# Optimization experiments

Hardware: AMD Instinct MI355X
Metric: run time of the kernel (lower is better)

Reference implementation:

```python
import jax, jax.numpy as jnp
import numpy as np


def setup_inputs() -> dict:
    key = jax.random.key(0)
    ks = jax.random.split(key, 8)
    B, T, V, H = 32, 256, 1024, 1024
    scale_i = 1.0 / np.sqrt(V)   # lecun_normal-style init for dense kernels
    scale_h = 1.0 / np.sqrt(H)
    return {
        "c0": jax.random.normal(ks[0], (B, H), jnp.float32),
        "h0": jax.random.normal(ks[1], (B, H), jnp.float32),
        "inputs": jax.random.normal(ks[2], (B, T, V), jnp.float32),
        "Wi": jax.random.normal(ks[3], (V, 4 * H), jnp.float32) * scale_i,
        "Wh": jax.random.normal(ks[4], (H, 4 * H), jnp.float32) * scale_h,
        "b": jnp.zeros((4 * H,), jnp.float32),
        "Wd": jax.random.normal(ks[5], (H, V), jnp.float32) * scale_h,
        "bd": jnp.zeros((V,), jnp.float32),
    }


def reference(c0, h0, inputs, Wi, Wh, b, Wd, bd):
    # LSTM scanned over time axis (axis=1 of inputs), then Dense -> vocab.
    H = h0.shape[-1]

    def step(carry, x_t):  # x_t: [B, V]
        c, h = carry
        z = x_t @ Wi + h @ Wh + b            # [B, 4H], gates i,f,g,o
        i, f, g, o = jnp.split(z, 4, axis=-1)
        i = jax.nn.sigmoid(i)
        f = jax.nn.sigmoid(f)
        g = jnp.tanh(g)
        o = jax.nn.sigmoid(o)
        c = f * c + i * g
        h = o * jnp.tanh(c)
        return (c, h), h

    xs = jnp.swapaxes(inputs, 0, 1)          # [T, B, V]
    (c, h), hs = jax.lax.scan(step, (c0, h0), xs)
    outputs = jnp.swapaxes(hs, 0, 1)          # [B, T, H]
    x = outputs @ Wd + bd                     # [B, T, V]
    return (c, h, x)
```

## Files before the change

### kernel.cpp

```cpp
#include <hip/hip_runtime.h>
#include <cstdio>

typedef unsigned short u16;
typedef unsigned int u32;
typedef unsigned long long u64;
typedef __attribute__((ext_vector_type(8))) short bf16x8;
typedef __attribute__((ext_vector_type(4))) float f32x4;

#define NWG 128

__device__ inline u16 f2bf(float x) {
  union { float f; unsigned u; } v; v.f = x;
  unsigned r = v.u + 0x7FFFu + ((v.u >> 16) & 1u);
  return (u16)(r >> 16);
}
__device__ inline float sigm(float x) { return 1.0f / (1.0f + __expf(-x)); }
__device__ inline float tanh_fast(float x) { return 1.0f - 2.0f / (__expf(2.0f * x) + 1.0f); }

__global__ __launch_bounds__(256) void k_convert(const float* __restrict__ in,
                                                 u16* __restrict__ out, int n4) {
  int i = blockIdx.x * blockDim.x + threadIdx.x;
  int stride = gridDim.x * blockDim.x;
  const float4* in4 = (const float4*)in;
  ushort4* out4 = (ushort4*)out;
  for (; i < n4; i += stride) {
    float4 v = in4[i];
    ushort4 o; o.x = f2bf(v.x); o.y = f2bf(v.y); o.z = f2bf(v.z); o.w = f2bf(v.w);
    out4[i] = o;
  }
}

__global__ __launch_bounds__(256) void k_init_h(const float* __restrict__ h0,
                                                u16* __restrict__ h_bf,
                                                u32* __restrict__ flags) {
  int i = blockIdx.x * blockDim.x + threadIdx.x;
  if (i < NWG) flags[i] = 0u;
  if (i < 32768) h_bf[i] = f2bf(h0[i]);
}

__global__ __launch_bounds__(256) void k_transpose(const float* __restrict__ in,
                                                   u16* __restrict__ out, int R, int C) {
  __shared__ u16 tile[32][33];
  int tx = threadIdx.x & 31, ty = threadIdx.x >> 5;
  int c = blockIdx.x * 32 + tx;
  for (int i = 0; i < 32; i += 8) {
    int r = blockIdx.y * 32 + ty + i;
    tile[ty + i][tx] = f2bf(in[(size_t)r * C + c]);
  }
  __syncthreads();
  int r = blockIdx.y * 32 + tx;
  for (int i = 0; i < 32; i += 8) {
    int cc = blockIdx.x * 32 + ty + i;
    out[(size_t)cc * R + r] = tile[tx][ty + i];
  }
}

__global__ __launch_bounds__(256) void k_gemm_bt(const u16* __restrict__ A,
                                                 const u16* __restrict__ BT,
                                                 const float* __restrict__ bias,
                                                 float* __restrict__ C,
                                                 int M, int N, int K) {
  __shared__ u16 As[128][40];
  __shared__ u16 Bs[128][40];
  const int m0 = blockIdx.y * 128, n0 = blockIdx.x * 128;
  const int tid = threadIdx.x;
  const int lane = tid & 63, wave = tid >> 6;
  const int wm = (wave >> 1) * 64, wn = (wave & 1) * 64;
  const int lm = lane & 15, quad = lane >> 4;
  const int r = tid >> 1, kh = (tid & 1) * 16;

  f32x4 acc[4][4];
  for (int i = 0; i < 4; i++)
    for (int j = 0; j < 4; j++) acc[i][j] = (f32x4){0.f, 0.f, 0.f, 0.f};

  for (int k0 = 0; k0 < K; k0 += 32) {
    const uint4* ap = (const uint4*)(A + (size_t)(m0 + r) * K + k0 + kh);
    uint4 av0 = ap[0], av1 = ap[1];
    const uint4* bp = (const uint4*)(BT + (size_t)(n0 + r) * K + k0 + kh);
    uint4 bv0 = bp[0], bv1 = bp[1];
    __syncthreads();
    *(uint4*)&As[r][kh] = av0; *(uint4*)&As[r][kh + 8] = av1;
    *(uint4*)&Bs[r][kh] = bv0; *(uint4*)&Bs[r][kh + 8] = bv1;
    __syncthreads();
    bf16x8 a_frag[4], b_frag[4];
    for (int i = 0; i < 4; i++) a_frag[i] = *(const bf16x8*)&As[wm + i * 16 + lm][quad * 8];
    for (int j = 0; j < 4; j++) b_frag[j] = *(const bf16x8*)&Bs[wn + j * 16 + lm][quad * 8];
    for (int i = 0; i < 4; i++)
      for (int j = 0; j < 4; j++)
        acc[i][j] = __builtin_amdgcn_mfma_f32_16x16x32_bf16(a_frag[i], b_frag[j], acc[i][j], 0, 0, 0);
  }
  for (int i = 0; i < 4; i++)
    for (int j = 0; j < 4; j++) {
      int row = m0 + wm + i * 16 + quad * 4;
      int col = n0 + wn + j * 16 + lm;
      float bc = bias[col];
      for (int rr = 0; rr < 4; rr++)
        C[(size_t)(row + rr) * N + col] = acc[i][j][rr] + bc;
    }
}

__global__ __launch_bounds__(256) void k_lstm(const float* __restrict__ Z,
                                              const u16* __restrict__ WhT,
                                              const float* __restrict__ c0,
                                              u16* __restrict__ h_bf,
                                              u16* __restrict__ Hs,
                                              float* __restrict__ out_c,
                                              float* __restrict__ out_h,
                                              u32* __restrict__ flags) {
  __shared__ u16 Whs[32][1032];
  __shared__ u16 h_lds[32][1032];
  __shared__ float z_buf[32][34];
  const int g = blockIdx.x;
  const int tid = threadIdx.x;
  const int lane = tid & 63, wave = tid >> 6;
  const int lm = lane & 15, quad = lane >> 4;
  const int mhalf = wave >> 1, ntile = wave & 1;
  const int b = tid >> 3, jl = tid & 7;

  {
    int pc = tid >> 3, seg = tid & 7;
    int grow = (pc >> 3) * 1024 + 8 * g + (pc & 7);
    const uint4* src = (const uint4*)(WhT + (size_t)grow * 1024 + seg * 128);
#pragma unroll
    for (int i = 0; i < 16; i++) {
      uint4 v = src[i];
      *(uint4*)&Whs[pc][seg * 128 + i * 8] = v;
    }
  }
  float creg = c0[b * 1024 + 8 * g + jl];

  for (int t = 0; t < 256; t++) {
    size_t zbase = ((size_t)b * 256 + t) * 4096 + 8 * g + jl;
    float z_i = Z[zbase], z_f = Z[zbase + 1024], z_g = Z[zbase + 2048], z_o = Z[zbase + 3072];

    {
      const u32 tgt = (u32)t;
      const u32* f0 = flags + lane;
      const u32* f1 = flags + 64 + lane;
      while (true) {
        u32 v0 = __hip_atomic_load(f0, __ATOMIC_RELAXED, __HIP_MEMORY_SCOPE_AGENT);
        u32 v1 = __hip_atomic_load(f1, __ATOMIC_RELAXED, __HIP_MEMORY_SCOPE_AGENT);
        if (__all((v0 >= tgt) && (v1 >= tgt))) break;
        __builtin_amdgcn_s_sleep(1);
      }
      asm volatile("" ::: "memory");
    }

    {
      const u64* hq = (const u64*)(h_bf + (size_t)(t & 1) * 32768);
      u64 v[32];
#pragma unroll
      for (int i = 0; i < 32; i++)
        v[i] = __hip_atomic_load(hq + i * 256 + tid, __ATOMIC_RELAXED, __HIP_MEMORY_SCOPE_AGENT);
#pragma unroll
      for (int i = 0; i < 32; i++) {
        int q = i * 256 + tid;
        *(u64*)&h_lds[q >> 8][(q & 255) * 4] = v[i];
      }
    }
    __syncthreads();

    const u16* arow = &h_lds[mhalf * 16 + lm][quad * 8];
    const u16* brow = &Whs[ntile * 16 + lm][quad * 8];
    f32x4 a0 = (f32x4){0.f, 0.f, 0.f, 0.f}, a1 = a0, a2 = a0, a3 = a0;
#pragma unroll
    for (int ks = 0; ks < 32; ks += 4) {
      bf16x8 af0 = *(const bf16x8*)(arow + (ks + 0) * 32);
      bf16x8 bf0 = *(const bf16x8*)(brow + (ks + 0) * 32);
      bf16x8 af1 = *(const bf16x8*)(arow + (ks + 1) * 32);
      bf16x8 bf1 = *(const bf16x8*)(brow + (ks + 1) * 32);
      bf16x8 af2 = *(const bf16x8*)(arow + (ks + 2) * 32);
      bf16x8 bf2 = *(const bf16x8*)(brow + (ks + 2) * 32);
      bf16x8 af3 = *(const bf16x8*)(arow + (ks + 3) * 32);
      bf16x8 bf3 = *(const bf16x8*)(brow + (ks + 3) * 32);
      a0 = __builtin_amdgcn_mfma_f32_16x16x32_bf16(af0, bf0, a0, 0, 0, 0);
      a1 = __builtin_amdgcn_mfma_f32_16x16x32_bf16(af1, bf1, a1, 0, 0, 0);
      a2 = __builtin_amdgcn_mfma_f32_16x16x32_bf16(af2, bf2, a2, 0, 0, 0);
      a3 = __builtin_amdgcn_mfma_f32_16x16x32_bf16(af3, bf3, a3, 0, 0, 0);
    }
    f32x4 accs = (a0 + a1) + (a2 + a3);
    for (int rr = 0; rr < 4; rr++)
      z_buf[mhalf * 16 + quad * 4 + rr][ntile * 16 + lm] = accs[rr];
    __syncthreads();

    float zi = z_buf[b][jl]      + z_i;
    float zf = z_buf[b][8 + jl]  + z_f;
    float zg = z_buf[b][16 + jl] + z_g;
    float zo = z_buf[b][24 + jl] + z_o;
    float ig = sigm(zi), fg = sigm(zf), gg = tanh_fast(zg), og = sigm(zo);
    creg = fg * creg + ig * gg;
    float hv = og * tanh_fast(creg);
    u16 hb = f2bf(hv);
    __hip_atomic_store(h_bf + (size_t)((t + 1) & 1) * 32768 + b * 1024 + 8 * g + jl,
                       hb, __ATOMIC_RELAXED, __HIP_MEMORY_SCOPE_AGENT);
    __syncthreads();
    if (tid == 0)
      __hip_atomic_store(flags + g, (u32)(t + 1),
                         __ATOMIC_RELAXED, __HIP_MEMORY_SCOPE_AGENT);

    __builtin_nontemporal_store(hb, Hs + ((size_t)b * 256 + t) * 1024 + 8 * g + jl);
    if (t == 255) {
      out_c[b * 1024 + 8 * g + jl] = creg;
      out_h[b * 1024 + 8 * g + jl] = hv;
    }
  }
}

extern "C" void kernel_launch(void* const* d_in, const int* in_sizes, int n_in,
                              void* d_out, int out_size, void* d_ws, size_t ws_size,
                              hipStream_t stream) {
  const float* c0   = (const float*)d_in[0];
  const float* h0   = (const float*)d_in[1];
  const float* X    = (const float*)d_in[2];
  const float* Wi   = (const float*)d_in[3];
  const float* Wh   = (const float*)d_in[4];
  const float* bias = (const float*)d_in[5];
  const float* Wd   = (const float*)d_in[6];
  const float* bd   = (const float*)d_in[7];
  float* out   = (float*)d_out;
  float* out_c = out;
  float* out_h = out + 32768;
  float* out_x = out + 65536;

  char* ws = (char*)d_ws;
  size_t off = 0;
  auto alloc = [&](size_t bytes) { char* p = ws + off; off += (bytes + 255) & ~255ull; return p; };
  float* Z     = (float*)alloc(134217728ull);
  u16*   Xb    = (u16*)alloc(16777216ull);
  u16*   WiT   = (u16*)alloc(8388608ull);
  u16*   WhT   = (u16*)alloc(8388608ull);
  u16*   WdT   = (u16*)alloc(2097152ull);
  u16*   Hs    = (u16*)alloc(16777216ull);
  u16*   h_bf  = (u16*)alloc(131072ull);
  u32*   flags = (u32*)alloc(NWG * 4);
  if (off > ws_size) {
    fprintf(stderr, "WS too small: need %zu have %zu\n", off, ws_size);
    return;
  }

  k_convert<<<2048, 256, 0, stream>>>(X, Xb, 8388608 / 4);
  k_init_h<<<128, 256, 0, stream>>>(h0, h_bf, flags);
  k_transpose<<<dim3(128, 32), 256, 0, stream>>>(Wi, WiT, 1024, 4096);
  k_transpose<<<dim3(128, 32), 256, 0, stream>>>(Wh, WhT, 1024, 4096);
  k_transpose<<<dim3(32, 32), 256, 0, stream>>>(Wd, WdT, 1024, 1024);
  k_gemm_bt<<<dim3(32, 64), 256, 0, stream>>>(Xb, WiT, bias, Z, 8192, 4096, 1024);
  k_lstm<<<NWG, 256, 0, stream>>>(Z, WhT, c0, h_bf, Hs, out_c, out_h, flags);
  k_gemm_bt<<<dim3(8, 64), 256, 0, stream>>>(Hs, WdT, bd, out_x, 8192, 1024, 1024);
}
```

Measured before the change: 1.188 ms.

## Halve persistent LSTM workgroups and keep recurrent weights in registers

The persistent recurrent kernel now runs 64 workgroups of 512 threads instead of 128 of 256, so each group owns 16 hidden units per gate. Each wave loads its slice of the recurrent weight matrix once into registers (32 bf16x8 fragments) instead of staging it in shared memory. This halves the number of flags polled in the per-step grid barrier and removes the per-step LDS reads of weights. In exchange it uses fewer CUs, raises register pressure with possible spills at 512 threads, and doubles the per-group MFMA work on the serial critical path.

```diff
diff --git a/kernel.cpp b/kernel.cpp
--- a/kernel.cpp
+++ b/kernel.cpp
@@ -7,7 +7,7 @@
 typedef __attribute__((ext_vector_type(8))) short bf16x8;
 typedef __attribute__((ext_vector_type(4))) float f32x4;
 
-#define NWG 128
+#define NWG 64
 
 __device__ inline u16 f2bf(float x) {
   union { float f; unsigned u; } v; v.f = x;
@@ -99,7 +99,7 @@
     }
 }
 
-__global__ __launch_bounds__(256) void k_lstm(const float* __restrict__ Z,
+__global__ __launch_bounds__(512) void k_lstm(const float* __restrict__ Z,
                                               const u16* __restrict__ WhT,
                                               const float* __restrict__ c0,
                                               u16* __restrict__ h_bf,
@@ -107,40 +107,35 @@
                                               float* __restrict__ out_c,
                                               float* __restrict__ out_h,
                                               u32* __restrict__ flags) {
-  __shared__ u16 Whs[32][1032];
   __shared__ u16 h_lds[32][1032];
-  __shared__ float z_buf[32][34];
+  __shared__ float z_buf[32][66];
   const int g = blockIdx.x;
   const int tid = threadIdx.x;
   const int lane = tid & 63, wave = tid >> 6;
   const int lm = lane & 15, quad = lane >> 4;
-  const int mhalf = wave >> 1, ntile = wave & 1;
-  const int b = tid >> 3, jl = tid & 7;
-
+  const int mhalf = wave >> 2;
+  const int nt = wave & 3;
+  const int b = tid >> 4, jl = tid & 15;
+
+  bf16x8 bfr[32];
   {
-    int pc = tid >> 3, seg = tid & 7;
-    int grow = (pc >> 3) * 1024 + 8 * g + (pc & 7);
-    const uint4* src = (const uint4*)(WhT + (size_t)grow * 1024 + seg * 128);
-#pragma unroll
-    for (int i = 0; i < 16; i++) {
-      uint4 v = src[i];
-      *(uint4*)&Whs[pc][seg * 128 + i * 8] = v;
-    }
-  }
-  float creg = c0[b * 1024 + 8 * g + jl];
+    const u16* wbase = WhT + (size_t)(nt * 1024 + 16 * g + lm) * 1024 + quad * 8;
+#pragma unroll
+    for (int ks = 0; ks < 32; ks++)
+      bfr[ks] = *(const bf16x8*)(wbase + ks * 32);
+  }
+  float creg = c0[b * 1024 + 16 * g + jl];
 
   for (int t = 0; t < 256; t++) {
-    size_t zbase = ((size_t)b * 256 + t) * 4096 + 8 * g + jl;
+    size_t zbase = ((size_t)b * 256 + t) * 4096 + 16 * g + jl;
     float z_i = Z[zbase], z_f = Z[zbase + 1024], z_g = Z[zbase + 2048], z_o = Z[zbase + 3072];
 
     {
       const u32 tgt = (u32)t;
       const u32* f0 = flags + lane;
-      const u32* f1 = flags + 64 + lane;
       while (true) {
         u32 v0 = __hip_atomic_load(f0, __ATOMIC_RELAXED, __HIP_MEMORY_SCOPE_AGENT);
-        u32 v1 = __hip_atomic_load(f1, __ATOMIC_RELAXED, __HIP_MEMORY_SCOPE_AGENT);
-        if (__all((v0 >= tgt) && (v1 >= tgt))) break;
+        if (__all(v0 >= tgt)) break;
         __builtin_amdgcn_s_sleep(1);
       }
       asm volatile("" ::: "memory");
@@ -148,60 +143,55 @@
 
     {
       const u64* hq = (const u64*)(h_bf + (size_t)(t & 1) * 32768);
-      u64 v[32];
-#pragma unroll
-      for (int i = 0; i < 32; i++)
-        v[i] = __hip_atomic_load(hq + i * 256 + tid, __ATOMIC_RELAXED, __HIP_MEMORY_SCOPE_AGENT);
-#pragma unroll
-      for (int i = 0; i < 32; i++) {
-        int q = i * 256 + tid;
-        *(u64*)&h_lds[q >> 8][(q & 255) * 4] = v[i];
+      u64 v[16];
+#pragma unroll
+      for (int i = 0; i < 16; i++)
+        v[i] = __hip_atomic_load(hq + i * 512 + tid, __ATOMIC_RELAXED, __HIP_MEMORY_SCOPE_AGENT);
+#pragma unroll
+      for (int i = 0; i < 16; i++) {
+        int bb = 2 * i + (tid >> 8);
+        *(u64*)&h_lds[bb][(tid & 255) * 4] = v[i];
       }
     }
     __syncthreads();
 
     const u16* arow = &h_lds[mhalf * 16 + lm][quad * 8];
-    const u16* brow = &Whs[ntile * 16 + lm][quad * 8];
     f32x4 a0 = (f32x4){0.f, 0.f, 0.f, 0.f}, a1 = a0, a2 = a0, a3 = a0;
 #pragma unroll
     for (int ks = 0; ks < 32; ks += 4) {
       bf16x8 af0 = *(const bf16x8*)(arow + (ks + 0) * 32);
-      bf16x8 bf0 = *(const bf16x8*)(brow + (ks + 0) * 32);
       bf16x8 af1 = *(const bf16x8*)(arow + (ks + 1) * 32);
-      bf16x8 bf1 = *(const bf16x8*)(brow + (ks + 1) * 32);
       bf16x8 af2 = *(const bf16x8*)(arow + (ks + 2) * 32);
-      bf16x8 bf2 = *(const bf16x8*)(brow + (ks + 2) * 32);
       bf16x8 af3 = *(const bf16x8*)(arow + (ks + 3) * 32);
-      bf16x8 bf3 = *(const bf16x8*)(brow + (ks + 3) * 32);
-      a0 = __builtin_amdgcn_mfma_f32_16x16x32_bf16(af0, bf0, a0, 0, 0, 0);
-      a1 = __builtin_amdgcn_mfma_f32_16x16x32_bf16(af1, bf1, a1, 0, 0, 0);
-      a2 = __builtin_amdgcn_mfma_f32_16x16x32_bf16(af2, bf2, a2, 0, 0, 0);
-      a3 = __builtin_amdgcn_mfma_f32_16x16x32_bf16(af3, bf3, a3, 0, 0, 0);
+      a0 = __builtin_amdgcn_mfma_f32_16x16x32_bf16(af0, bfr[ks + 0], a0, 0, 0, 0);
+      a1 = __builtin_amdgcn_mfma_f32_16x16x32_bf16(af1, bfr[ks + 1], a1, 0, 0, 0);
+      a2 = __builtin_amdgcn_mfma_f32_16x16x32_bf16(af2, bfr[ks + 2], a2, 0, 0, 0);
+      a3 = __builtin_amdgcn_mfma_f32_16x16x32_bf16(af3, bfr[ks + 3], a3, 0, 0, 0);
     }
     f32x4 accs = (a0 + a1) + (a2 + a3);
     for (int rr = 0; rr < 4; rr++)
-      z_buf[mhalf * 16 + quad * 4 + rr][ntile * 16 + lm] = accs[rr];
+      z_buf[mhalf * 16 + quad * 4 + rr][nt * 16 + lm] = accs[rr];
     __syncthreads();
 
     float zi = z_buf[b][jl]      + z_i;
-    float zf = z_buf[b][8 + jl]  + z_f;
-    float zg = z_buf[b][16 + jl] + z_g;
-    float zo = z_buf[b][24 + jl] + z_o;
+    float zf = z_buf[b][16 + jl] + z_f;
+    float zg = z_buf[b][32 + jl] + z_g;
+    float zo = z_buf[b][48 + jl] + z_o;
     float ig = sigm(zi), fg = sigm(zf), gg = tanh_fast(zg), og = sigm(zo);
     creg = fg * creg + ig * gg;
     float hv = og * tanh_fast(creg);
     u16 hb = f2bf(hv);
-    __hip_atomic_store(h_bf + (size_t)((t + 1) & 1) * 32768 + b * 1024 + 8 * g + jl,
+    __hip_atomic_store(h_bf + (size_t)((t + 1) & 1) * 32768 + b * 1024 + 16 * g + jl,
                        hb, __ATOMIC_RELAXED, __HIP_MEMORY_SCOPE_AGENT);
     __syncthreads();
     if (tid == 0)
       __hip_atomic_store(flags + g, (u32)(t + 1),
                          __ATOMIC_RELAXED, __HIP_MEMORY_SCOPE_AGENT);
 
-    __builtin_nontemporal_store(hb, Hs + ((size_t)b * 256 + t) * 1024 + 8 * g + jl);
+    __builtin_nontemporal_store(hb, Hs + ((size_t)b * 256 + t) * 1024 + 16 * g + jl);
     if (t == 255) {
-      out_c[b * 1024 + 8 * g + jl] = creg;
-      out_h[b * 1024 + 8 * g + jl] = hv;
+      out_c[b * 1024 + 16 * g + jl] = creg;
+      out_h[b * 1024 + 16 * g + jl] = hv;
     }
   }
 }
@@ -244,6 +234,6 @@
   k_transpose<<<dim3(128, 32), 256, 0, stream>>>(Wh, WhT, 1024, 4096);
   k_transpose<<<dim3(32, 32), 256, 0, stream>>>(Wd, WdT, 1024, 1024);
   k_gemm_bt<<<dim3(32, 64), 256, 0, stream>>>(Xb, WiT, bias, Z, 8192, 4096, 1024);
-  k_lstm<<<NWG, 256, 0, stream>>>(Z, WhT, c0, h_bf, Hs, out_c, out_h, flags);
+  k_lstm<<<NWG, 512, 0, stream>>>(Z, WhT, c0, h_bf, Hs, out_c, out_h, flags);
   k_gemm_bt<<<dim3(8, 64), 256, 0, stream>>>(Hs, WdT, bd, out_x, 8192, 1024, 1024);
 }
```

After: 1.427 ms. +20.1%, slower.
